# Optimization experiments

Measured on AMD Instinct MI355X. Metric: run time of the kernel, lower is better.

The kernel has to match this reference:

```python
import jax, jax.numpy as jnp
import numpy as np

NUM_GRAPHS = 1000


def gcn_conv(x, src, dst, n_nodes, W, b):
    """PyG GCNConv: symmetric normalization with self-loops, then scatter-add."""
    # self-loops already appended to src/dst by caller
    deg = jax.ops.segment_sum(jnp.ones_like(dst, dtype=x.dtype), dst, num_segments=n_nodes)
    dinv = jnp.where(deg > 0, jax.lax.rsqrt(deg), 0.0)
    norm = dinv[src] * dinv[dst]                      # [E+N]
    h = x @ W.T                                       # [N, out]
    msg = h[src] * norm[:, None]                      # gather + scale
    out = jax.ops.segment_sum(msg, dst, num_segments=n_nodes)
    return out + b


def setup_inputs() -> dict:
    key = jax.random.key(0)
    ks = jax.random.split(key, 9)
    N, E = 100000, 1600000
    x = jax.random.normal(ks[0], (N, 32), dtype=jnp.float32)
    edge_index = jax.random.randint(ks[1], (2, E), 0, N, dtype=jnp.int64)
    batch = jnp.sort(jax.random.randint(ks[2], (N,), 0, NUM_GRAPHS, dtype=jnp.int64))
    # parameters (Glorot-ish scale)
    W1 = jax.random.normal(ks[3], (16, 32), dtype=jnp.float32) * (1.0 / np.sqrt(32))
    b1 = jnp.zeros((16,), dtype=jnp.float32)
    W2 = jax.random.normal(ks[4], (16, 16), dtype=jnp.float32) * (1.0 / np.sqrt(16))
    b2 = jnp.zeros((16,), dtype=jnp.float32)
    Wl = jax.random.normal(ks[5], (5, 16), dtype=jnp.float32) * (1.0 / np.sqrt(16))
    bl = jnp.zeros((5,), dtype=jnp.float32)
    return {"x": x, "edge_index": edge_index, "batch": batch,
            "W1": W1, "b1": b1, "W2": W2, "b2": b2, "Wl": Wl, "bl": bl}


def reference(x, edge_index, batch, W1, b1, W2, b2, Wl, bl):
    n_nodes = x.shape[0]
    loops = jnp.arange(n_nodes, dtype=edge_index.dtype)
    src = jnp.concatenate([edge_index[0], loops])
    dst = jnp.concatenate([edge_index[1], loops])

    h = gcn_conv(x, src, dst, n_nodes, W1, b1)
    h = jax.nn.relu(h)
    h = gcn_conv(h, src, dst, n_nodes, W2, b2)

    # global mean pool over graphs
    sums = jax.ops.segment_sum(h, batch, num_segments=NUM_GRAPHS)
    cnts = jax.ops.segment_sum(jnp.ones((n_nodes,), dtype=h.dtype), batch, num_segments=NUM_GRAPHS)
    pooled = sums / jnp.maximum(cnts, 1.0)[:, None]   # [G, 16]

    logits = pooled @ Wl.T + bl                       # [G, 5]
    return jax.nn.softmax(logits, axis=-1)
```

## Files before the change

### kernel.cpp

```cpp
#include <hip/hip_runtime.h>
#include <hip/hip_fp16.h>
#include <math.h>

#define NG 1000
#define NPN 512
#define PSH 9
#define MAXPART 256
#define K1BLK 256

__global__ void zero_kernel(int4* __restrict__ p, int n4) {
    int i = blockIdx.x * blockDim.x + threadIdx.x;
    if (i < n4) p[i] = make_int4(0, 0, 0, 0);
}

__global__ void __launch_bounds__(256) pcount_kernel(const int* __restrict__ dst,
                                                     int* __restrict__ pcnt,
                                                     int E, int CH, int NPART) {
    __shared__ int h[MAXPART];
    int b = blockIdx.x, t = threadIdx.x;
    h[t] = 0;
    __syncthreads();
    int beg = b * CH, end = min(E, beg + CH);
    for (int e = beg + t; e < end; e += 256) atomicAdd(&h[dst[e] >> PSH], 1);
    __syncthreads();
    if (t < NPART && h[t] > 0) atomicAdd(&pcnt[t], h[t]);
}

__global__ void __launch_bounds__(256) pscan_kernel(const int* __restrict__ pcnt,
                                                    int* __restrict__ poff,
                                                    int* __restrict__ pcur,
                                                    int* __restrict__ rowptr,
                                                    int NPART, int N, int E) {
    __shared__ int sm[256];
    int t = threadIdx.x;
    int v = (t < NPART) ? pcnt[t] : 0;
    sm[t] = v;
    __syncthreads();
    for (int o = 1; o < 256; o <<= 1) {
        int u = (t >= o) ? sm[t - o] : 0;
        __syncthreads();
        sm[t] += u;
        __syncthreads();
    }
    int ex = sm[t] - v;
    if (t < NPART) { poff[t] = ex; pcur[t] = ex; }
    if (t == NPART - 1) poff[NPART] = ex + v;
    if (t == 0) rowptr[N] = E;
}

__global__ void __launch_bounds__(256) pscatter_kernel(const int* __restrict__ src,
                                                       const int* __restrict__ dst,
                                                       int* __restrict__ pcur,
                                                       int* __restrict__ ibuf,
                                                       int E, int CH, int NPART) {
    __shared__ int h[MAXPART];
    __shared__ int gbase[MAXPART];
    int b = blockIdx.x, t = threadIdx.x;
    h[t] = 0;
    __syncthreads();
    int beg = b * CH, end = min(E, beg + CH);
    for (int e = beg + t; e < end; e += 256) atomicAdd(&h[dst[e] >> PSH], 1);
    __syncthreads();
    if (t < NPART) gbase[t] = (h[t] > 0) ? atomicAdd(&pcur[t], h[t]) : 0;
    __syncthreads();
    h[t] = 0;
    __syncthreads();
    for (int e = beg + t; e < end; e += 256) {
        int s = src[e], d = dst[e];
        int p = d >> PSH;
        int pos = gbase[p] + atomicAdd(&h[p], 1);
        ibuf[pos] = ((d & (NPN - 1)) << 17) | s;
    }
}

__global__ void __launch_bounds__(256) part_kernel(const int* __restrict__ poff,
                                                   const int* __restrict__ ibuf,
                                                   int* __restrict__ csr,
                                                   int* __restrict__ rowptr,
                                                   float* __restrict__ dinv,
                                                   const float* __restrict__ X,
                                                   const float* __restrict__ W1,
                                                   __half* __restrict__ A1h, int N) {
    __shared__ int h[NPN];
    __shared__ int ex[NPN];
    __shared__ int cur[NPN];
    __shared__ int sm[256];
    __shared__ float sW1[512];
    int p = blockIdx.x, t = threadIdx.x;
    int base = p * NPN;
    for (int k = t; k < NPN; k += 256) h[k] = 0;
    sW1[t] = W1[t];
    sW1[t + 256] = W1[t + 256];
    __syncthreads();
    int ebeg = poff[p], eend = poff[p + 1];
    for (int e = ebeg + t; e < eend; e += 256) atomicAdd(&h[ibuf[e] >> 17], 1);
    __syncthreads();
    int a0 = h[2 * t], a1 = h[2 * t + 1];
    int s = a0 + a1;
    sm[t] = s;
    __syncthreads();
    for (int o = 1; o < 256; o <<= 1) {
        int u = (t >= o) ? sm[t - o] : 0;
        __syncthreads();
        sm[t] += u;
        __syncthreads();
    }
    int exc = sm[t] - s;
    ex[2 * t] = exc;          cur[2 * t] = exc;
    ex[2 * t + 1] = exc + a0; cur[2 * t + 1] = exc + a0;
    __syncthreads();
    for (int k = t; k < NPN; k += 256) {
        int n = base + k;
        if (n < N) {
            rowptr[n] = ebeg + ex[k];
            dinv[n] = rsqrtf((float)h[k] + 1.0f);
        }
    }
    for (int e = ebeg + t; e < eend; e += 256) {
        int w = ibuf[e];
        int ln = w >> 17;
        int pos = ebeg + atomicAdd(&cur[ln], 1);
        csr[pos] = w & 0x1FFFF;
    }
    for (int k = t; k < NPN; k += 256) {
        int n = base + k;
        if (n >= N) continue;
        float dd = rsqrtf((float)h[k] + 1.0f);
        float xv[32];
        const float4* xp = (const float4*)(X + (size_t)n * 32);
#pragma unroll
        for (int qq = 0; qq < 8; qq++) {
            float4 v = xp[qq];
            xv[4*qq+0] = v.x; xv[4*qq+1] = v.y; xv[4*qq+2] = v.z; xv[4*qq+3] = v.w;
        }
        union { __half2 h2[8]; uint4 u4[2]; } pk;
#pragma unroll
        for (int j2 = 0; j2 < 8; j2++) {
            float o[2];
#pragma unroll
            for (int jj = 0; jj < 2; jj++) {
                int j = j2 * 2 + jj;
                float a = 0.f;
#pragma unroll
                for (int kk = 0; kk < 32; kk++) a += xv[kk] * sW1[j * 32 + kk];
                o[jj] = a * dd;
            }
            pk.h2[j2] = __floats2half2_rn(o[0], o[1]);
        }
        uint4* yp = (uint4*)(A1h + (size_t)n * 16);
        yp[0] = pk.u4[0];
        yp[1] = pk.u4[1];
    }
}

__device__ __forceinline__ void add8(float* a, uint4 v) {
    float2 f;
    f = __half22float2(*(const __half2*)&v.x); a[0] += f.x; a[1] += f.y;
    f = __half22float2(*(const __half2*)&v.y); a[2] += f.x; a[3] += f.y;
    f = __half22float2(*(const __half2*)&v.z); a[4] += f.x; a[5] += f.y;
    f = __half22float2(*(const __half2*)&v.w); a[6] += f.x; a[7] += f.y;
}

__global__ void __launch_bounds__(256) agg1_kernel(
    const int* __restrict__ rowptr, const int* __restrict__ csr,
    const float* __restrict__ dinv, const __half* __restrict__ A1h,
    const float* __restrict__ b1, const float* __restrict__ W2,
    __half* __restrict__ A2h, int N) {
    __shared__ float sW2[256];
    __shared__ float sb1[16];
    __shared__ float tile[128][17];
    int t = threadIdx.x;
    int team = t >> 1, q = t & 1;
    int node = blockIdx.x * 128 + team;
    sW2[t] = W2[t];
    if (t < 16) sb1[t] = b1[t];
    __syncthreads();
    const uint4* H4 = (const uint4*)A1h;
    float dd = 0.f;
    if (node < N) {
        dd = dinv[node];
        float acc[8] = {0.f,0.f,0.f,0.f,0.f,0.f,0.f,0.f};
        add8(acc, H4[(size_t)node * 2 + q]);
        int e = rowptr[node], end = rowptr[node + 1];
        for (; e + 3 < end; e += 4) {
            int s0 = csr[e], s1 = csr[e+1], s2 = csr[e+2], s3 = csr[e+3];
            uint4 g0 = H4[(size_t)s0 * 2 + q];
            uint4 g1 = H4[(size_t)s1 * 2 + q];
            uint4 g2 = H4[(size_t)s2 * 2 + q];
            uint4 g3 = H4[(size_t)s3 * 2 + q];
            add8(acc, g0); add8(acc, g1); add8(acc, g2); add8(acc, g3);
        }
        for (; e < end; e++) add8(acc, H4[(size_t)csr[e] * 2 + q]);
#pragma unroll
        for (int j = 0; j < 8; j++)
            tile[team][q * 8 + j] = fmaxf(acc[j] * dd + sb1[q * 8 + j], 0.f);
    }
    __syncthreads();
    if (node < N) {
        float o[8];
#pragma unroll
        for (int jj = 0; jj < 8; jj++) {
            int j = q * 8 + jj;
            float a = 0.f;
#pragma unroll
            for (int k = 0; k < 16; k++) a += tile[team][k] * sW2[j * 16 + k];
            o[jj] = a * dd;
        }
        uint4 ov;
        ((__half2*)&ov)[0] = __floats2half2_rn(o[0], o[1]);
        ((__half2*)&ov)[1] = __floats2half2_rn(o[2], o[3]);
        ((__half2*)&ov)[2] = __floats2half2_rn(o[4], o[5]);
        ((__half2*)&ov)[3] = __floats2half2_rn(o[6], o[7]);
        ((uint4*)A2h)[(size_t)node * 2 + q] = ov;
    }
}

__global__ void __launch_bounds__(256) agg2_kernel(
    const int* __restrict__ rowptr, const int* __restrict__ csr,
    const float* __restrict__ dinv, const __half* __restrict__ A2h,
    const int* __restrict__ batch, float* __restrict__ pooled,
    float* __restrict__ cnt, int N) {
    __shared__ float tile[128][17];
    __shared__ int gb[128];
    int t = threadIdx.x;
    int team = t >> 1, q = t & 1;
    int base = blockIdx.x * 128;
    int node = base + team;
    if (t < 128) {
        int n = base + t;
        gb[t] = (n < N) ? batch[n] : -1;
    }
    const uint4* H4 = (const uint4*)A2h;
    if (node < N) {
        float dd = dinv[node];
        float acc[8] = {0.f,0.f,0.f,0.f,0.f,0.f,0.f,0.f};
        add8(acc, H4[(size_t)node * 2 + q]);
        int e = rowptr[node], end = rowptr[node + 1];
        for (; e + 3 < end; e += 4) {
            int s0 = csr[e], s1 = csr[e+1], s2 = csr[e+2], s3 = csr[e+3];
            uint4 g0 = H4[(size_t)s0 * 2 + q];
            uint4 g1 = H4[(size_t)s1 * 2 + q];
            uint4 g2 = H4[(size_t)s2 * 2 + q];
            uint4 g3 = H4[(size_t)s3 * 2 + q];
            add8(acc, g0); add8(acc, g1); add8(acc, g2); add8(acc, g3);
        }
        for (; e < end; e++) add8(acc, H4[(size_t)csr[e] * 2 + q]);
#pragma unroll
        for (int j = 0; j < 8; j++) tile[team][q * 8 + j] = acc[j] * dd;
    }
    __syncthreads();
    int nmax = N - base; if (nmax > 128) nmax = 128;
    if (t < 16 && nmax > 0) {
        int c = t;
        int g = gb[0];
        float a = 0.f, k = 0.f;
        for (int n = 0; n < nmax; n++) {
            int gi = gb[n];
            if (gi != g) {
                atomicAdd(&pooled[(size_t)g * 16 + c], a);
                if (c == 0) atomicAdd(&cnt[g], k);
                a = 0.f; k = 0.f; g = gi;
            }
            a += tile[n][c];
            k += 1.f;
        }
        atomicAdd(&pooled[(size_t)g * 16 + c], a);
        if (c == 0) atomicAdd(&cnt[g], k);
    }
}

__global__ void head_kernel(const float* __restrict__ pooled, const float* __restrict__ cnt,
                            const float* __restrict__ b2, const float* __restrict__ Wl,
                            const float* __restrict__ bl, float* __restrict__ out) {
    int g = blockIdx.x * blockDim.x + threadIdx.x;
    if (g >= NG) return;
    float c = cnt[g];
    c = c > 1.0f ? c : 1.0f;
    float inv = 1.0f / c;
    float p[16];
#pragma unroll
    for (int j = 0; j < 16; j++) p[j] = pooled[(size_t)g * 16 + j] * inv + b2[j];
    float logits[5], m = -INFINITY;
#pragma unroll
    for (int r = 0; r < 5; r++) {
        float a = bl[r];
#pragma unroll
        for (int j = 0; j < 16; j++) a += p[j] * Wl[r * 16 + j];
        logits[r] = a;
        m = fmaxf(m, a);
    }
    float s = 0.f;
#pragma unroll
    for (int r = 0; r < 5; r++) { logits[r] = expf(logits[r] - m); s += logits[r]; }
    float is = 1.0f / s;
#pragma unroll
    for (int r = 0; r < 5; r++) out[(size_t)g * 5 + r] = logits[r] * is;
}

static inline size_t rnd16b(size_t bytes) { return (bytes + 15) & ~(size_t)15; }

extern "C" void kernel_launch(void* const* d_in, const int* in_sizes, int n_in,
                              void* d_out, int out_size, void* d_ws, size_t ws_size,
                              hipStream_t stream) {
    const float* x     = (const float*)d_in[0];
    const int*   edge  = (const int*)d_in[1];
    const int*   batch = (const int*)d_in[2];
    const float* W1    = (const float*)d_in[3];
    const float* b1    = (const float*)d_in[4];
    const float* W2    = (const float*)d_in[5];
    const float* b2    = (const float*)d_in[6];
    const float* Wl    = (const float*)d_in[7];
    const float* bl    = (const float*)d_in[8];

    const int N = in_sizes[0] / 32;
    const int E = in_sizes[1] / 2;
    const int* src = edge;
    const int* dst = edge + E;

    const int NPART = (N + NPN - 1) / NPN;
    const int CH = (E + K1BLK - 1) / K1BLK;

    char* ws = (char*)d_ws;
    size_t off = 0;
    int*      pcnt   = (int*)(ws + off);      off += rnd16b((size_t)MAXPART * 4);
    float*    pooled = (float*)(ws + off);    off += rnd16b((size_t)NG * 16 * 4);
    float*    cnt    = (float*)(ws + off);    off += rnd16b((size_t)NG * 4);
    size_t zbytes = off;
    int*      poff   = (int*)(ws + off);      off += rnd16b((size_t)(MAXPART + 1) * 4);
    int*      pcur   = (int*)(ws + off);      off += rnd16b((size_t)MAXPART * 4);
    int*      rowptr = (int*)(ws + off);      off += rnd16b((size_t)(N + 1) * 4);
    float*    dinv   = (float*)(ws + off);    off += rnd16b((size_t)N * 4);
    int*      ibuf   = (int*)(ws + off);      off += rnd16b((size_t)E * 4);
    int*      csr    = (int*)(ws + off);      off += rnd16b((size_t)E * 4);
    __half*   A1h    = (__half*)(ws + off);   off += rnd16b((size_t)N * 16 * 2);
    __half*   A2h    = (__half*)(ws + off);   off += rnd16b((size_t)N * 16 * 2);

    int n4 = (int)(zbytes / 16);
    zero_kernel<<<(n4 + 255) / 256, 256, 0, stream>>>((int4*)d_ws, n4);

    pcount_kernel<<<K1BLK, 256, 0, stream>>>(dst, pcnt, E, CH, NPART);
    pscan_kernel<<<1, 256, 0, stream>>>(pcnt, poff, pcur, rowptr, NPART, N, E);
    pscatter_kernel<<<K1BLK, 256, 0, stream>>>(src, dst, pcur, ibuf, E, CH, NPART);
    part_kernel<<<NPART, 256, 0, stream>>>(poff, ibuf, csr, rowptr, dinv, x, W1, A1h, N);

    int gAgg = (N + 127) / 128;
    agg1_kernel<<<gAgg, 256, 0, stream>>>(rowptr, csr, dinv, A1h, b1, W2, A2h, N);
    agg2_kernel<<<gAgg, 256, 0, stream>>>(rowptr, csr, dinv, A2h, batch, pooled, cnt, N);
    head_kernel<<<(NG + 255) / 256, 256, 0, stream>>>(pooled, cnt, b2, Wl, bl, (float*)d_out);
}
```

Before: 118.4 us.

## Replace atomic partition counting with per-block histograms and scan

The histogram kernel now writes a per-block partition histogram and also zeroes the workspace, which removes the separate zero kernel launch. A single-block scan computes per-block base offsets for each partition. The scatter kernel then uses those precomputed offsets and no longer recounts the dst histogram or takes global atomics. This removes one kernel launch and a second pass over dst. The cost is a serial scan of 256 block entries per thread in one block, plus extra workspace for the histograms and offsets.

```diff
diff --git a/kernel.cpp b/kernel.cpp
--- a/kernel.cpp
+++ b/kernel.cpp
@@ -8,33 +8,36 @@
 #define MAXPART 256
 #define K1BLK 256
 
-__global__ void zero_kernel(int4* __restrict__ p, int n4) {
-    int i = blockIdx.x * blockDim.x + threadIdx.x;
-    if (i < n4) p[i] = make_int4(0, 0, 0, 0);
-}
-
-__global__ void __launch_bounds__(256) pcount_kernel(const int* __restrict__ dst,
-                                                     int* __restrict__ pcnt,
-                                                     int E, int CH, int NPART) {
+__global__ void __launch_bounds__(256) hist_kernel(const int* __restrict__ dst,
+                                                   int* __restrict__ bhist,
+                                                   int4* __restrict__ zero4, int z4,
+                                                   int E, int CH) {
     __shared__ int h[MAXPART];
     int b = blockIdx.x, t = threadIdx.x;
     h[t] = 0;
+    int gid = b * 256 + t;
+    if (gid < z4) zero4[gid] = make_int4(0, 0, 0, 0);
     __syncthreads();
     int beg = b * CH, end = min(E, beg + CH);
     for (int e = beg + t; e < end; e += 256) atomicAdd(&h[dst[e] >> PSH], 1);
     __syncthreads();
-    if (t < NPART && h[t] > 0) atomicAdd(&pcnt[t], h[t]);
-}
-
-__global__ void __launch_bounds__(256) pscan_kernel(const int* __restrict__ pcnt,
-                                                    int* __restrict__ poff,
-                                                    int* __restrict__ pcur,
-                                                    int* __restrict__ rowptr,
-                                                    int NPART, int N, int E) {
+    bhist[b * MAXPART + t] = h[t];
+}
+
+__global__ void __launch_bounds__(256) scan_kernel(const int* __restrict__ bhist,
+                                                   int* __restrict__ gbase,
+                                                   int* __restrict__ poff,
+                                                   int* __restrict__ rowptr,
+                                                   int NPART, int N, int E) {
     __shared__ int sm[256];
     int t = threadIdx.x;
-    int v = (t < NPART) ? pcnt[t] : 0;
-    sm[t] = v;
+    int running = 0;
+    for (int b = 0; b < K1BLK; b++) {
+        int v = bhist[b * MAXPART + t];
+        gbase[b * MAXPART + t] = running;
+        running += v;
+    }
+    sm[t] = running;
     __syncthreads();
     for (int o = 1; o < 256; o <<= 1) {
         int u = (t >= o) ? sm[t - o] : 0;
@@ -42,33 +45,27 @@
         sm[t] += u;
         __syncthreads();
     }
-    int ex = sm[t] - v;
-    if (t < NPART) { poff[t] = ex; pcur[t] = ex; }
-    if (t == NPART - 1) poff[NPART] = ex + v;
+    int ex = sm[t] - running;
+    if (t < NPART) poff[t] = ex;
+    if (t == NPART - 1) poff[NPART] = ex + running;
     if (t == 0) rowptr[N] = E;
 }
 
-__global__ void __launch_bounds__(256) pscatter_kernel(const int* __restrict__ src,
-                                                       const int* __restrict__ dst,
-                                                       int* __restrict__ pcur,
-                                                       int* __restrict__ ibuf,
-                                                       int E, int CH, int NPART) {
-    __shared__ int h[MAXPART];
-    __shared__ int gbase[MAXPART];
+__global__ void __launch_bounds__(256) scatter_kernel(const int* __restrict__ src,
+                                                      const int* __restrict__ dst,
+                                                      const int* __restrict__ poff,
+                                                      const int* __restrict__ gbase,
+                                                      int* __restrict__ ibuf,
+                                                      int E, int CH, int NPART) {
+    __shared__ int cur[MAXPART];
     int b = blockIdx.x, t = threadIdx.x;
-    h[t] = 0;
+    if (t < NPART) cur[t] = poff[t] + gbase[b * MAXPART + t];
     __syncthreads();
     int beg = b * CH, end = min(E, beg + CH);
-    for (int e = beg + t; e < end; e += 256) atomicAdd(&h[dst[e] >> PSH], 1);
-    __syncthreads();
-    if (t < NPART) gbase[t] = (h[t] > 0) ? atomicAdd(&pcur[t], h[t]) : 0;
-    __syncthreads();
-    h[t] = 0;
-    __syncthreads();
     for (int e = beg + t; e < end; e += 256) {
         int s = src[e], d = dst[e];
         int p = d >> PSH;
-        int pos = gbase[p] + atomicAdd(&h[p], 1);
+        int pos = atomicAdd(&cur[p], 1);
         ibuf[pos] = ((d & (NPN - 1)) << 17) | s;
     }
 }
@@ -322,25 +319,24 @@
 
     char* ws = (char*)d_ws;
     size_t off = 0;
-    int*      pcnt   = (int*)(ws + off);      off += rnd16b((size_t)MAXPART * 4);
     float*    pooled = (float*)(ws + off);    off += rnd16b((size_t)NG * 16 * 4);
     float*    cnt    = (float*)(ws + off);    off += rnd16b((size_t)NG * 4);
     size_t zbytes = off;
     int*      poff   = (int*)(ws + off);      off += rnd16b((size_t)(MAXPART + 1) * 4);
-    int*      pcur   = (int*)(ws + off);      off += rnd16b((size_t)MAXPART * 4);
     int*      rowptr = (int*)(ws + off);      off += rnd16b((size_t)(N + 1) * 4);
     float*    dinv   = (float*)(ws + off);    off += rnd16b((size_t)N * 4);
+    int*      bhist  = (int*)(ws + off);      off += rnd16b((size_t)K1BLK * MAXPART * 4);
+    int*      gbase  = (int*)(ws + off);      off += rnd16b((size_t)K1BLK * MAXPART * 4);
     int*      ibuf   = (int*)(ws + off);      off += rnd16b((size_t)E * 4);
     int*      csr    = (int*)(ws + off);      off += rnd16b((size_t)E * 4);
     __half*   A1h    = (__half*)(ws + off);   off += rnd16b((size_t)N * 16 * 2);
     __half*   A2h    = (__half*)(ws + off);   off += rnd16b((size_t)N * 16 * 2);
 
-    int n4 = (int)(zbytes / 16);
-    zero_kernel<<<(n4 + 255) / 256, 256, 0, stream>>>((int4*)d_ws, n4);
-
-    pcount_kernel<<<K1BLK, 256, 0, stream>>>(dst, pcnt, E, CH, NPART);
-    pscan_kernel<<<1, 256, 0, stream>>>(pcnt, poff, pcur, rowptr, NPART, N, E);
-    pscatter_kernel<<<K1BLK, 256, 0, stream>>>(src, dst, pcur, ibuf, E, CH, NPART);
+    int z4 = (int)(zbytes / 16);
+
+    hist_kernel<<<K1BLK, 256, 0, stream>>>(dst, bhist, (int4*)d_ws, z4, E, CH);
+    scan_kernel<<<1, 256, 0, stream>>>(bhist, gbase, poff, rowptr, NPART, N, E);
+    scatter_kernel<<<K1BLK, 256, 0, stream>>>(src, dst, poff, gbase, ibuf, E, CH, NPART);
     part_kernel<<<NPART, 256, 0, stream>>>(poff, ibuf, csr, rowptr, dinv, x, W1, A1h, N);
 
     int gAgg = (N + 127) / 128;
```

Measured after the change: 109.1 us. 1.09x faster.
